# Performance work log

Hardware: AMD Instinct MI355X
Metric: run time of the kernel (lower is better)

## Reference

```python
import jax, jax.numpy as jnp
import numpy as np
from jax import lax

WEIGHT = 1.0
NUM_DILATION_STEPS = 20
FAR_DIST = 20.0


def _neighbor_count(x, kernel, num_classes):
    # grouped 3x3 conv with center tap zeroed, SAME padding (stride 1)
    return lax.conv_general_dilated(
        x, kernel, window_strides=(1, 1), padding='SAME',
        feature_group_count=num_classes,
        dimension_numbers=('NCHW', 'OIHW', 'NCHW'))


def fast_sdf(target_mask, num_classes):
    # target_mask: [B, H, W] int labels -> per-class chamfer-ish distance map [B, C, H, W]
    one_hot = jnp.transpose(jax.nn.one_hot(target_mask, num_classes, dtype=jnp.float32),
                            (0, 3, 1, 2))  # [B, C, H, W]
    foreground = (one_hot > 0.5).astype(jnp.float32)

    # 3x3 all-ones kernel with center zero, one per class (grouped conv)
    k = np.ones((num_classes, 1, 3, 3), dtype=np.float32)
    k[:, 0, 1, 1] = 0.0
    kernel = jnp.asarray(k)

    dist_map0 = jnp.zeros_like(foreground)

    def step(i, state):
        dist_map, current_mask = state
        dilated = (_neighbor_count(current_mask, kernel, num_classes) > 0).astype(jnp.float32)
        # note: faithful to torch code -- pixels with no neighbors vanish and
        # contribute negative increments, exactly as `dilated - current_mask` does
        new_pixels = dilated - current_mask
        dist_map = dist_map + new_pixels * (i + 1).astype(jnp.float32)
        return (dist_map, dilated)

    dist_map, current_mask = lax.fori_loop(0, NUM_DILATION_STEPS, step,
                                           (dist_map0, foreground))
    return jnp.where(current_mask == 0, FAR_DIST, dist_map)


def setup_inputs() -> dict:
    key = jax.random.key(0)
    k1, k2 = jax.random.split(key)
    B, C, H, W = 8, 19, 512, 512
    pred = jax.random.normal(k1, (B, C, H, W), dtype=jnp.float32)
    target = jax.random.randint(k2, (B, H, W), 0, C, dtype=jnp.int64)
    return {"pred": pred, "target": target}


def reference(pred, target):
    num_classes = pred.shape[1]
    probs = jax.nn.softmax(pred, axis=1)
    gt_sdf = lax.stop_gradient(fast_sdf(target, num_classes))
    loss = jnp.mean(probs * gt_sdf)
    return WEIGHT * loss
```

## Files before the change

kernel.cpp:

```cpp
#include <hip/hip_runtime.h>

#define B_ 8
#define C_ 19
#define H_ 512
#define W_ 512
#define HW_ (H_*W_)

#define HALO   20
#define SINT   56
#define SROWS  96
#define NSTRIP 10
#define LSTR   9

typedef unsigned long long u64;

__global__ __launch_bounds__(256) void mask_kernel(const int* __restrict__ target,
                                                   u64* __restrict__ masks) {
    __shared__ u64 mlds[128][21];
    const int blk  = blockIdx.x;
    const int b    = blk >> 5;
    const int base = (blk & 31) * 128;
    const int tid  = threadIdx.x;
    const int lane = tid & 63, wv = tid >> 6;
    const int* tgt = target + b * HW_;
    for (int t = 0; t < 32; ++t) {
        const int cl = wv * 32 + t;
        const int x  = tgt[(base + cl) * 64 + lane];
        u64 keep = 0;
        #pragma unroll
        for (int c = 0; c < C_; ++c) {
            u64 m = __ballot(x == c);
            if (lane == c) keep = m;
        }
        if (lane < C_) mlds[cl][lane] = keep;
    }
    __syncthreads();
    for (int idx = tid; idx < C_ * 128; idx += 256) {
        const int c = idx >> 7, wl = idx & 127;
        masks[((size_t)b * C_ + c) * 4096 + base + wl] = mlds[wl][c];
    }
}

__global__ __launch_bounds__(256) void invd_kernel(const float* __restrict__ pred,
                                                   float* __restrict__ invd) {
    const int t   = blockIdx.x * 256 + threadIdx.x;
    const int b   = t >> 16;
    const int hw4 = (t & 65535) << 2;
    const float* pbase = pred + (size_t)b * C_ * HW_ + hw4;
    float s0=0.f, s1=0.f, s2=0.f, s3=0.f;
    #pragma unroll
    for (int c = 0; c < C_; ++c) {
        float4 v = *(const float4*)(pbase + (size_t)c * HW_);
        s0 += __expf(v.x); s1 += __expf(v.y); s2 += __expf(v.z); s3 += __expf(v.w);
    }
    float4 o; o.x = 1.0f/s0; o.y = 1.0f/s1; o.z = 1.0f/s2; o.w = 1.0f/s3;
    *(float4*)(invd + (size_t)b * HW_ + hw4) = o;
}

__global__ __launch_bounds__(256) void sdf_loss_kernel(const u64* __restrict__ masks,
                                                       const float* __restrict__ pred,
                                                       const float* __restrict__ invd,
                                                       float* __restrict__ out) {
    __shared__ u64 bufA[SROWS * LSTR];
    __shared__ u64 bufB[SROWS * LSTR];
    __shared__ int chg[2];
    __shared__ float part[4];
    const int blk   = blockIdx.x;
    const int strip = blk % NSTRIP;
    const int bc    = blk / NSTRIP;
    const int b     = bc / C_;
    const int c     = bc - b * C_;
    const int y0    = strip * SINT;
    const int tid   = threadIdx.x;
    const u64* mk   = masks + ((size_t)b * C_ + c) * 4096;

    if (tid < 2) chg[tid] = 0;

    for (int idx = tid; idx < SROWS * 8; idx += 256) {
        const int lr = idx >> 3, wq = idx & 7;
        const int gy = y0 - HALO + lr;
        u64 m = 0;
        if (gy >= 0 && gy < H_) m = mk[gy * 8 + wq];
        bufA[lr * LSTR + wq] = m;
    }
    __syncthreads();

    const int w  = tid & 7;
    const int r0 = (tid >> 3) * 3;

    u64 cnt[3][5];
    u64 iso[3];
    u64 save[3];
    #pragma unroll
    for (int i = 0; i < 3; ++i) {
        iso[i] = 0; save[i] = 0;
        #pragma unroll
        for (int j = 0; j < 5; ++j) cnt[i][j] = 0;
    }

    u64* cur = bufA;
    u64* nxt = bufB;
    int  Kleft;
    bool conv = false;

    {
        u64 h[5], nc[5], ccm[5];
        #pragma unroll
        for (int j = 0; j < 5; ++j) {
            const int r = r0 - 1 + j;
            u64 C = 0, L = 0, R = 0;
            if (r >= 0 && r < SROWS) {
                const u64* p = cur + r * LSTR + w;
                C = p[0];
                L = w ? p[-1] : 0;
                R = (w < 7) ? p[1] : 0;
            }
            nc[j]  = (C << 1) | (L >> 63) | (C >> 1) | (R << 63);
            h[j]   = nc[j] | C;
            ccm[j] = C;
        }
        u64 diff = 0;
        #pragma unroll
        for (int i = 0; i < 3; ++i) {
            const u64 cc  = ccm[i + 1];
            const u64 nbr = nc[i + 1] | h[i] | h[i + 2];
            const u64 d   = cc | nbr;
            iso[i] = cc & ~nbr;
            diff |= d ^ cc;
            u64 carry = ~cc;
            #pragma unroll
            for (int j = 0; j < 5; ++j) { u64 t = cnt[i][j] & carry; cnt[i][j] ^= carry; carry = t; }
            save[i] = d;
            nxt[(r0 + i) * LSTR + w] = d;
        }
        if (diff) chg[1] = 1;
        if (tid == 0) chg[0] = 0;
        __syncthreads();
        if (!chg[1]) { Kleft = 19; conv = true; }
        else { u64* t = cur; cur = nxt; nxt = t; }
    }

    if (!conv) {
        for (int s = 2; s <= 19; ++s) {
            u64 h[5], ccm[3];
            #pragma unroll
            for (int j = 0; j < 5; ++j) {
                const int r = r0 - 1 + j;
                u64 C = 0, L = 0, R = 0;
                if (r >= 0 && r < SROWS) {
                    const u64* p = cur + r * LSTR + w;
                    C = p[0];
                    L = w ? p[-1] : 0;
                    R = (w < 7) ? p[1] : 0;
                }
                h[j] = C | (C << 1) | (L >> 63) | (C >> 1) | (R << 63);
                if (j >= 1 && j <= 3) ccm[j - 1] = C;
            }
            u64 diff = 0;
            #pragma unroll
            for (int i = 0; i < 3; ++i) {
                const u64 cc = ccm[i];
                const u64 d  = h[i] | h[i + 1] | h[i + 2];
                diff |= d ^ cc;
                u64 carry = ~cc;
                #pragma unroll
                for (int j = 0; j < 5; ++j) { u64 t = cnt[i][j] & carry; cnt[i][j] ^= carry; carry = t; }
                save[i] = d;
                nxt[(r0 + i) * LSTR + w] = d;
            }
            if (diff) chg[s & 1] = 1;
            if (tid == 0) chg[(s + 1) & 1] = 0;
            __syncthreads();
            if (!chg[s & 1]) { Kleft = 20 - s; conv = true; break; }
            u64* t = cur; cur = nxt; nxt = t;
        }
        if (!conv) Kleft = 1;
    }

    #pragma unroll
    for (int i = 0; i < 3; ++i) {
        const u64 m = ~save[i];
        u64 carry = 0;
        #pragma unroll
        for (int j = 0; j < 5; ++j) {
            const u64 a  = ((Kleft >> j) & 1) ? m : 0;
            const u64 x  = cnt[i][j];
            const u64 s1 = x ^ a;
            const u64 c1 = x & a;
            cnt[i][j] = s1 ^ carry;
            carry = c1 | (s1 & carry);
        }
    }

    float acc = 0.f;
    #pragma unroll
    for (int i = 0; i < 3; ++i) {
        const int lr = r0 + i;
        const int gy = y0 - HALO + lr;
        if (lr < HALO || lr >= HALO + SINT || gy >= H_) continue;
        cnt[i][0] |= iso[i];
        u64 q[8];
        #pragma unroll
        for (int g = 0; g < 8; ++g) {
            u64 x = 0;
            #pragma unroll
            for (int j = 0; j < 5; ++j)
                x |= ((cnt[i][j] >> (8 * g)) & 0xFFULL) << (8 * j);
            u64 t;
            t = (x ^ (x >> 7))  & 0x00AA00AA00AA00AAULL; x ^= t ^ (t << 7);
            t = (x ^ (x >> 14)) & 0x0000CCCC0000CCCCULL; x ^= t ^ (t << 14);
            t = (x ^ (x >> 28)) & 0x00000000F0F0F0F0ULL; x ^= t ^ (t << 28);
            q[g] = x;
        }
        const float4* pp = (const float4*)(pred + ((size_t)b * C_ + c) * HW_ + gy * W_ + w * 64);
        const float4* dd = (const float4*)(invd + (size_t)b * HW_ + gy * W_ + w * 64);
        #pragma unroll
        for (int k = 0; k < 16; ++k) {
            const float4 v  = pp[k];
            const float4 dv = dd[k];
            const u64 qq = q[k >> 1];
            const int sh = (k & 1) * 32;
            acc = fmaf(__expf(v.x) * dv.x, (float)(unsigned)((qq >> (sh     )) & 0xFF), acc);
            acc = fmaf(__expf(v.y) * dv.y, (float)(unsigned)((qq >> (sh +  8)) & 0xFF), acc);
            acc = fmaf(__expf(v.z) * dv.z, (float)(unsigned)((qq >> (sh + 16)) & 0xFF), acc);
            acc = fmaf(__expf(v.w) * dv.w, (float)(unsigned)((qq >> (sh + 24)) & 0xFF), acc);
        }
    }

    #pragma unroll
    for (int off = 32; off > 0; off >>= 1) acc += __shfl_down(acc, off);
    if ((tid & 63) == 0) part[tid >> 6] = acc;
    __syncthreads();
    if (tid == 0) {
        float s = (part[0] + part[1]) + (part[2] + part[3]);
        atomicAdd(out, s * (1.0f / 39845888.0f));
    }
}

extern "C" void kernel_launch(void* const* d_in, const int* in_sizes, int n_in,
                              void* d_out, int out_size, void* d_ws, size_t ws_size,
                              hipStream_t stream) {
    const float* pred   = (const float*)d_in[0];
    const int*   target = (const int*)d_in[1];
    float* invd = (float*)d_ws;
    u64*   masks = (u64*)((char*)d_ws + 8388608);
    float* out = (float*)d_out;

    hipMemsetAsync(out, 0, sizeof(float), stream);
    mask_kernel<<<256, 256, 0, stream>>>(target, masks);
    invd_kernel<<<2048, 256, 0, stream>>>(pred, invd);
    sdf_loss_kernel<<<B_ * C_ * NSTRIP, 256, 0, stream>>>(masks, pred, invd, out);
}
```

Before: 325.9 us.

## Keep dilation rows in registers and encode distances as step bit-planes

The SDF loss kernel now loads each thread's own three mask rows straight into registers. Left and right boundary bits come from warp shuffles, and only the horizontally dilated rows go to shared memory, so each step reads just two halo rows from LDS instead of fifteen words. The per-step ripple-carry counter and the final Kleft addition are replaced by OR-ing each newly reached pixel into the bit-planes of its step index, with never-reached pixels set to 20 directly. The dilation loop is fully unrolled, and the mask-building kernel is split into twice as many smaller blocks. This trades some extra shuffles and register pressure for fewer LDS reads and less bit-arithmetic per step.

```diff
diff --git a/kernel.cpp b/kernel.cpp
--- a/kernel.cpp
+++ b/kernel.cpp
@@ -16,15 +16,15 @@
 
 __global__ __launch_bounds__(256) void mask_kernel(const int* __restrict__ target,
                                                    u64* __restrict__ masks) {
-    __shared__ u64 mlds[128][21];
+    __shared__ u64 mlds[64][21];
     const int blk  = blockIdx.x;
-    const int b    = blk >> 5;
-    const int base = (blk & 31) * 128;
+    const int b    = blk >> 6;
+    const int base = (blk & 63) * 64;
     const int tid  = threadIdx.x;
     const int lane = tid & 63, wv = tid >> 6;
     const int* tgt = target + b * HW_;
-    for (int t = 0; t < 32; ++t) {
-        const int cl = wv * 32 + t;
+    for (int t = 0; t < 16; ++t) {
+        const int cl = wv * 16 + t;
         const int x  = tgt[(base + cl) * 64 + lane];
         u64 keep = 0;
         #pragma unroll
@@ -35,8 +35,8 @@
         if (lane < C_) mlds[cl][lane] = keep;
     }
     __syncthreads();
-    for (int idx = tid; idx < C_ * 128; idx += 256) {
-        const int c = idx >> 7, wl = idx & 127;
+    for (int idx = tid; idx < C_ * 64; idx += 256) {
+        const int c = idx >> 6, wl = idx & 63;
         masks[((size_t)b * C_ + c) * 4096 + base + wl] = mlds[wl][c];
     }
 }
@@ -72,123 +72,113 @@
     const int c     = bc - b * C_;
     const int y0    = strip * SINT;
     const int tid   = threadIdx.x;
+    const int w     = tid & 7;
+    const int r0    = (tid >> 3) * 3;
     const u64* mk   = masks + ((size_t)b * C_ + c) * 4096;
 
     if (tid < 2) chg[tid] = 0;
 
-    for (int idx = tid; idx < SROWS * 8; idx += 256) {
-        const int lr = idx >> 3, wq = idx & 7;
-        const int gy = y0 - HALO + lr;
-        u64 m = 0;
-        if (gy >= 0 && gy < H_) m = mk[gy * 8 + wq];
-        bufA[lr * LSTR + wq] = m;
+    u64 save[3], hreg[3], iso[3], pl[3][5];
+    #pragma unroll
+    for (int i = 0; i < 3; ++i) {
+        iso[i] = 0;
+        #pragma unroll
+        for (int j = 0; j < 5; ++j) pl[i][j] = 0;
+    }
+
+    #pragma unroll
+    for (int i = 0; i < 3; ++i) {
+        const int gy = y0 - HALO + r0 + i;
+        save[i] = (gy >= 0 && gy < H_) ? mk[gy * 8 + w] : 0;
+    }
+
+    u64 nc[3];
+    {
+        unsigned mp = (unsigned)(save[0] >> 63) | ((unsigned)(save[1] >> 63) << 1) | ((unsigned)(save[2] >> 63) << 2);
+        unsigned lp = ((unsigned)save[0] & 1) | (((unsigned)save[1] & 1) << 1) | (((unsigned)save[2] & 1) << 2);
+        unsigned fl = __shfl_up(mp, 1);   if (w == 0) fl = 0;
+        unsigned fr = __shfl_down(lp, 1); if (w == 7) fr = 0;
+        #pragma unroll
+        for (int i = 0; i < 3; ++i) {
+            nc[i]   = (save[i] << 1) | (save[i] >> 1) | (u64)((fl >> i) & 1) | ((u64)((fr >> i) & 1) << 63);
+            hreg[i] = nc[i] | save[i];
+            bufA[(r0 + i) * LSTR + w] = hreg[i];
+        }
     }
     __syncthreads();
-
-    const int w  = tid & 7;
-    const int r0 = (tid >> 3) * 3;
-
-    u64 cnt[3][5];
-    u64 iso[3];
-    u64 save[3];
-    #pragma unroll
-    for (int i = 0; i < 3; ++i) {
-        iso[i] = 0; save[i] = 0;
-        #pragma unroll
-        for (int j = 0; j < 5; ++j) cnt[i][j] = 0;
-    }
 
     u64* cur = bufA;
     u64* nxt = bufB;
-    int  Kleft;
-    bool conv = false;
+    bool done = false;
 
     {
-        u64 h[5], nc[5], ccm[5];
-        #pragma unroll
-        for (int j = 0; j < 5; ++j) {
-            const int r = r0 - 1 + j;
-            u64 C = 0, L = 0, R = 0;
-            if (r >= 0 && r < SROWS) {
-                const u64* p = cur + r * LSTR + w;
-                C = p[0];
-                L = w ? p[-1] : 0;
-                R = (w < 7) ? p[1] : 0;
-            }
-            nc[j]  = (C << 1) | (L >> 63) | (C >> 1) | (R << 63);
-            h[j]   = nc[j] | C;
-            ccm[j] = C;
-        }
+        u64 hup = (r0 > 0)          ? cur[(r0 - 1) * LSTR + w] : 0;
+        u64 hdn = (r0 + 3 < SROWS)  ? cur[(r0 + 3) * LSTR + w] : 0;
+        u64 nbr[3], d[3];
+        nbr[0] = nc[0] | hup     | hreg[1];
+        nbr[1] = nc[1] | hreg[0] | hreg[2];
+        nbr[2] = nc[2] | hreg[1] | hdn;
         u64 diff = 0;
         #pragma unroll
         for (int i = 0; i < 3; ++i) {
-            const u64 cc  = ccm[i + 1];
-            const u64 nbr = nc[i + 1] | h[i] | h[i + 2];
-            const u64 d   = cc | nbr;
-            iso[i] = cc & ~nbr;
-            diff |= d ^ cc;
-            u64 carry = ~cc;
-            #pragma unroll
-            for (int j = 0; j < 5; ++j) { u64 t = cnt[i][j] & carry; cnt[i][j] ^= carry; carry = t; }
-            save[i] = d;
-            nxt[(r0 + i) * LSTR + w] = d;
+            iso[i] = save[i] & ~nbr[i];
+            d[i]   = save[i] | nbr[i];
+            u64 nb = d[i] ^ save[i];
+            pl[i][0] |= nb;
+            diff |= nb;
+            save[i] = d[i];
+        }
+        unsigned mp = (unsigned)(d[0] >> 63) | ((unsigned)(d[1] >> 63) << 1) | ((unsigned)(d[2] >> 63) << 2);
+        unsigned lp = ((unsigned)d[0] & 1) | (((unsigned)d[1] & 1) << 1) | (((unsigned)d[2] & 1) << 2);
+        unsigned fl = __shfl_up(mp, 1);   if (w == 0) fl = 0;
+        unsigned fr = __shfl_down(lp, 1); if (w == 7) fr = 0;
+        #pragma unroll
+        for (int i = 0; i < 3; ++i) {
+            hreg[i] = d[i] | (d[i] << 1) | (d[i] >> 1) | (u64)((fl >> i) & 1) | ((u64)((fr >> i) & 1) << 63);
+            nxt[(r0 + i) * LSTR + w] = hreg[i];
         }
         if (diff) chg[1] = 1;
         if (tid == 0) chg[0] = 0;
         __syncthreads();
-        if (!chg[1]) { Kleft = 19; conv = true; }
+        if (!chg[1]) done = true;
         else { u64* t = cur; cur = nxt; nxt = t; }
     }
 
-    if (!conv) {
+    if (!done) {
+        #pragma unroll
         for (int s = 2; s <= 19; ++s) {
-            u64 h[5], ccm[3];
-            #pragma unroll
-            for (int j = 0; j < 5; ++j) {
-                const int r = r0 - 1 + j;
-                u64 C = 0, L = 0, R = 0;
-                if (r >= 0 && r < SROWS) {
-                    const u64* p = cur + r * LSTR + w;
-                    C = p[0];
-                    L = w ? p[-1] : 0;
-                    R = (w < 7) ? p[1] : 0;
-                }
-                h[j] = C | (C << 1) | (L >> 63) | (C >> 1) | (R << 63);
-                if (j >= 1 && j <= 3) ccm[j - 1] = C;
-            }
+            u64 hup = (r0 > 0)         ? cur[(r0 - 1) * LSTR + w] : 0;
+            u64 hdn = (r0 + 3 < SROWS) ? cur[(r0 + 3) * LSTR + w] : 0;
+            u64 d[3];
+            d[0] = hup     | hreg[0] | hreg[1];
+            d[1] = hreg[0] | hreg[1] | hreg[2];
+            d[2] = hreg[1] | hreg[2] | hdn;
             u64 diff = 0;
             #pragma unroll
             for (int i = 0; i < 3; ++i) {
-                const u64 cc = ccm[i];
-                const u64 d  = h[i] | h[i + 1] | h[i + 2];
-                diff |= d ^ cc;
-                u64 carry = ~cc;
-                #pragma unroll
-                for (int j = 0; j < 5; ++j) { u64 t = cnt[i][j] & carry; cnt[i][j] ^= carry; carry = t; }
-                save[i] = d;
-                nxt[(r0 + i) * LSTR + w] = d;
+                u64 nb = d[i] ^ save[i];
+                diff |= nb;
+                if (s & 1)  pl[i][0] |= nb;
+                if (s & 2)  pl[i][1] |= nb;
+                if (s & 4)  pl[i][2] |= nb;
+                if (s & 8)  pl[i][3] |= nb;
+                if (s & 16) pl[i][4] |= nb;
+                save[i] = d[i];
+            }
+            unsigned mp = (unsigned)(d[0] >> 63) | ((unsigned)(d[1] >> 63) << 1) | ((unsigned)(d[2] >> 63) << 2);
+            unsigned lp = ((unsigned)d[0] & 1) | (((unsigned)d[1] & 1) << 1) | (((unsigned)d[2] & 1) << 2);
+            unsigned fl = __shfl_up(mp, 1);   if (w == 0) fl = 0;
+            unsigned fr = __shfl_down(lp, 1); if (w == 7) fr = 0;
+            #pragma unroll
+            for (int i = 0; i < 3; ++i) {
+                hreg[i] = d[i] | (d[i] << 1) | (d[i] >> 1) | (u64)((fl >> i) & 1) | ((u64)((fr >> i) & 1) << 63);
+                nxt[(r0 + i) * LSTR + w] = hreg[i];
             }
             if (diff) chg[s & 1] = 1;
             if (tid == 0) chg[(s + 1) & 1] = 0;
             __syncthreads();
-            if (!chg[s & 1]) { Kleft = 20 - s; conv = true; break; }
+            if (!chg[s & 1]) break;
             u64* t = cur; cur = nxt; nxt = t;
-        }
-        if (!conv) Kleft = 1;
-    }
-
-    #pragma unroll
-    for (int i = 0; i < 3; ++i) {
-        const u64 m = ~save[i];
-        u64 carry = 0;
-        #pragma unroll
-        for (int j = 0; j < 5; ++j) {
-            const u64 a  = ((Kleft >> j) & 1) ? m : 0;
-            const u64 x  = cnt[i][j];
-            const u64 s1 = x ^ a;
-            const u64 c1 = x & a;
-            cnt[i][j] = s1 ^ carry;
-            carry = c1 | (s1 & carry);
         }
     }
 
@@ -198,14 +188,17 @@
         const int lr = r0 + i;
         const int gy = y0 - HALO + lr;
         if (lr < HALO || lr >= HALO + SINT || gy >= H_) continue;
-        cnt[i][0] |= iso[i];
+        pl[i][0] |= iso[i];
+        const u64 m = ~save[i];
+        pl[i][2] |= m;
+        pl[i][4] |= m;
         u64 q[8];
         #pragma unroll
         for (int g = 0; g < 8; ++g) {
             u64 x = 0;
             #pragma unroll
             for (int j = 0; j < 5; ++j)
-                x |= ((cnt[i][j] >> (8 * g)) & 0xFFULL) << (8 * j);
+                x |= ((pl[i][j] >> (8 * g)) & 0xFFULL) << (8 * j);
             u64 t;
             t = (x ^ (x >> 7))  & 0x00AA00AA00AA00AAULL; x ^= t ^ (t << 7);
             t = (x ^ (x >> 14)) & 0x0000CCCC0000CCCCULL; x ^= t ^ (t << 14);
@@ -247,7 +240,7 @@
     float* out = (float*)d_out;
 
     hipMemsetAsync(out, 0, sizeof(float), stream);
-    mask_kernel<<<256, 256, 0, stream>>>(target, masks);
+    mask_kernel<<<512, 256, 0, stream>>>(target, masks);
     invd_kernel<<<2048, 256, 0, stream>>>(pred, invd);
     sdf_loss_kernel<<<B_ * C_ * NSTRIP, 256, 0, stream>>>(masks, pred, invd, out);
 }
```

Result: faster. 298.6 us (-8.4%).
